# Performance work log

Measured on AMD Instinct MI355X. Metric: run time of the kernel, lower is better.

Reference implementation:

```python
import jax, jax.numpy as jnp
import numpy as np

H = W = 160  # grid mesh -> N = 25600 vertices
B = 4
D = 64


def _grid_mesh(h, w):
    """Triangulated grid; returns symmetric directed edge list (e0, e1), lexicographically
    sorted like np.where(adj > 0) in the original module."""
    idx = np.arange(h * w).reshape(h, w)
    v00 = idx[:-1, :-1].ravel(); v01 = idx[:-1, 1:].ravel()
    v10 = idx[1:, :-1].ravel(); v11 = idx[1:, 1:].ravel()
    faces = np.concatenate([np.stack([v00, v01, v11], 1), np.stack([v00, v11, v10], 1)], 0)
    pairs = np.concatenate([faces[:, [0, 1]], faces[:, [1, 2]], faces[:, [0, 2]]], 0)
    pairs = np.concatenate([pairs, pairs[:, ::-1]], 0)  # symmetrize (adj + adj.T)
    pairs = np.unique(pairs, axis=0)
    return pairs[:, 0].astype(np.int32), pairs[:, 1].astype(np.int32)


def setup_inputs() -> dict:
    key = jax.random.key(0)
    k1, k2 = jax.random.split(key)
    N = H * W
    e0, e1 = _grid_mesh(H, W)
    x = jax.random.normal(k1, (B, N, 3), dtype=jnp.float32)
    J = jax.random.normal(k2, (B, 3 * N, D), dtype=jnp.float32)
    return {"x": x, "J": J, "e0": jnp.asarray(e0), "e1": jnp.asarray(e1), "k": 0}


def _skew(v):
    # cross-product matrix [v]_x : [E,3,3]
    z = jnp.zeros_like(v[:, 0])
    return jnp.stack([
        jnp.stack([z, -v[:, 2], v[:, 1]], -1),
        jnp.stack([v[:, 2], z, -v[:, 0]], -1),
        jnp.stack([-v[:, 1], v[:, 0], z], -1)], -2)


def _arap_single(xi, Ji, e0, e1, deg):
    N = xi.shape[0]
    Dd = Ji.shape[-1]
    J3 = Ji.reshape(N, 3, Dd)           # per-node 3xD blocks of J
    v = xi[e0] - xi[e1]                  # edge vectors [E,3]
    # (2L kron I3) @ J with L = D - A (edge weights 1), coalesce == scatter-add
    nb = jnp.zeros_like(J3).at[e0].add(J3[e1])
    LJ = 2.0 * (deg[:, None, None] * J3 - nb)
    JTLJ = jnp.einsum('ncd,nce->de', J3, LJ)
    # B has block [v]_x at (e0,e1) and accumulated [v]_x at (e0,e0); B^T blocks are -[v]_x
    S = _skew(v)                         # [E,3,3]
    SJ = jnp.einsum('eij,ejd->eid', S, J3[e0])
    BTJ = jnp.zeros_like(J3).at[e1].add(-SJ).at[e0].add(-SJ)
    # C: block-diagonal, per-node sum over outgoing edges of (|v|^2 I - v v^T), then 3x3 inverse
    I3 = jnp.eye(3, dtype=xi.dtype)
    Cb = (v * v).sum(-1)[:, None, None] * I3 - v[:, :, None] * v[:, None, :]
    C = jnp.zeros((N, 3, 3), xi.dtype).at[e0].add(Cb)
    Cinv = jnp.linalg.inv(C)
    CBTJ = jnp.einsum('nij,njd->nid', Cinv, BTJ)
    JTBCBTJ = jnp.einsum('ncd,nce->de', BTJ, CBTJ)
    e = jnp.clip(jnp.linalg.eigvalsh(JTLJ - JTBCBTJ), 0.0)
    pos = e > 0
    # sqrt(clip(e,0)) with a guard so the vjp stays finite at clipped zeros
    return jnp.where(pos, jnp.sqrt(jnp.where(pos, e, 1.0)), 0.0).sum()


def reference(x, J, e0, e1, k):
    N = x.shape[1]
    deg = jnp.zeros((N,), x.dtype).at[e0].add(1.0)
    traces = jax.vmap(lambda xi, Ji: _arap_single(xi, Ji, e0, e1, deg))(x, J)
    return traces.mean()
```

## Files before the change

### kernel.cpp

```cpp
#include <hip/hip_runtime.h>

constexpr int BN = 4;
constexpr int NV = 25600;
constexpr int DD = 64;
constexpr int PP = 72;
constexpr int KP = 34;
constexpr int WW = 160;
constexpr size_t GEOM_OFF = 1u << 20;
constexpr int GREC = 36;
constexpr int GXN  = 256;
constexpr int NCH  = NV / 4;
constexpr int NITER = NCH / GXN;
static_assert(NITER * GXN == NCH, "grid must divide chunks");

constexpr int NS_STEPS = 11;
__constant__ const float S_TAB[NS_STEPS]  = {1.999940f, 1.999730f, 1.998790f, 1.994560f,
                                             1.976020f, 1.900200f, 1.653000f, 1.241700f,
                                             1.024220f, 1.000220f, 1.000000f};
__constant__ const float MU_TAB[NS_STEPS] = {1.414192f, 1.414118f, 1.413786f, 1.412289f,
                                             1.405710f, 1.378478f, 1.285690f, 1.114316f,
                                             1.012038f, 1.000110f, 1.000000f};

typedef __attribute__((ext_vector_type(8))) short short8;
typedef __attribute__((ext_vector_type(4))) float floatx4;

__device__ __forceinline__ unsigned short f2bf(float x) {
    unsigned u = __float_as_uint(x);
    u += 0x7fffu + ((u >> 16) & 1u);
    return (unsigned short)(u >> 16);
}
__device__ __forceinline__ float bf2f(unsigned short h) {
    return __uint_as_float(((unsigned)h) << 16);
}
__device__ __forceinline__ unsigned pack2bf(float a, float b) {
    return (unsigned)f2bf(a) | ((unsigned)f2bf(b) << 16);
}

__global__ void rowptr_kernel(const int* __restrict__ e0, int E, int* __restrict__ row_ptr,
                              float* __restrict__ M, float* __restrict__ out) {
    int i = blockIdx.x * blockDim.x + threadIdx.x;
    if (i < BN * 64 * 64) M[i] = 0.f;
    if (i == 0) out[0] = 0.f;
    if (i > NV) return;
    int lo = 0, hi = E;
    while (lo < hi) {
        int mid = (lo + hi) >> 1;
        if (e0[mid] < i) lo = mid + 1; else hi = mid;
    }
    row_ptr[i] = lo;
}

__global__ __launch_bounds__(256) void geom_kernel(
    const float* __restrict__ x, float* __restrict__ geom,
    float* __restrict__ M, float* __restrict__ out)
{
    const int gid = blockIdx.x * 256 + threadIdx.x;
    if (gid < BN * 64 * 64) M[gid] = 0.f;
    if (gid == 0) out[0] = 0.f;
    if (gid >= BN * NV) return;
    const int b = gid / NV;
    const int n = gid - b * NV;
    const int r = n / WW;
    const int c = n - r * WW;
    const bool up = r > 0, dn = r < WW - 1, lf = c > 0, rt = c < WW - 1;
    int mm[6];
    mm[0] = (up && lf) ? n - WW - 1 : n;
    mm[1] = up ? n - WW : n;
    mm[2] = lf ? n - 1 : n;
    mm[3] = rt ? n + 1 : n;
    mm[4] = dn ? n + WW : n;
    mm[5] = (dn && rt) ? n + WW + 1 : n;

    const float* xb = x + (size_t)b * NV * 3;
    const float xn0 = xb[n * 3], xn1 = xb[n * 3 + 1], xn2 = xb[n * 3 + 2];
    float v[6][3];
    float sv0 = 0, sv1 = 0, sv2 = 0;
    float cxx = 0, cxy = 0, cxz = 0, cyy = 0, cyz = 0, czz = 0;
#pragma unroll
    for (int k = 0; k < 6; k++) {
        const int m = mm[k];
        const float v0 = xn0 - xb[m * 3];
        const float v1 = xn1 - xb[m * 3 + 1];
        const float v2 = xn2 - xb[m * 3 + 2];
        v[k][0] = v0; v[k][1] = v1; v[k][2] = v2;
        sv0 += v0; sv1 += v1; sv2 += v2;
        const float s2 = v0 * v0 + v1 * v1 + v2 * v2;
        cxx += s2 - v0 * v0; cyy += s2 - v1 * v1; czz += s2 - v2 * v2;
        cxy -= v0 * v1; cxz -= v0 * v2; cyz -= v1 * v2;
    }
    const float co00 = cyy * czz - cyz * cyz;
    const float co01 = cxz * cyz - cxy * czz;
    const float co02 = cxy * cyz - cxz * cyy;
    const float det  = cxx * co00 + cxy * co01 + cxz * co02;
    const float id   = 1.0f / det;
    const float i00 = co00 * id, i01 = co01 * id, i02 = co02 * id;
    const float i11 = (cxx * czz - cxz * cxz) * id;
    const float i12 = (cxz * cxy - cxx * cyz) * id;
    const float i22 = (cxx * cyy - cxy * cxy) * id;

    float4* g4 = (float4*)(geom + (size_t)gid * GREC);
    g4[0] = make_float4(v[0][0], v[0][1], v[0][2], v[1][0]);
    g4[1] = make_float4(v[1][1], v[1][2], v[2][0], v[2][1]);
    g4[2] = make_float4(v[2][2], v[3][0], v[3][1], v[3][2]);
    g4[3] = make_float4(v[4][0], v[4][1], v[4][2], v[5][0]);
    g4[4] = make_float4(v[5][1], v[5][2], sv0, sv1);
    g4[5] = make_float4(sv2, i00, i01, i02);
    g4[6] = make_float4(i11, i12, i22, 0.f);
    g4[7] = make_float4(__int_as_float(mm[0]), __int_as_float(mm[1]),
                        __int_as_float(mm[2]), __int_as_float(mm[3]));
    g4[8] = make_float4(__int_as_float(mm[4]), __int_as_float(mm[5]), 0.f, 0.f);
}

__device__ __forceinline__ short8 ldfrag(const unsigned short* a, int row, int quad) {
    const unsigned* p = (const unsigned*)(a + row * KP + quad * 8);
    union { unsigned u[4]; short8 s; } t;
    t.u[0] = p[0]; t.u[1] = p[1]; t.u[2] = p[2]; t.u[3] = p[3];
    return t.s;
}

struct GRec { float v[18]; float sv[3]; float ci[6]; int mm[6]; };
struct JRegs { float n0, n1, n2; float m0[6], m1[6], m2[6]; };

__device__ __forceinline__ void load_grec(const float* __restrict__ g, GRec& o) {
#pragma unroll
    for (int i = 0; i < 18; i++) o.v[i] = g[i];
    o.sv[0] = g[18]; o.sv[1] = g[19]; o.sv[2] = g[20];
#pragma unroll
    for (int i = 0; i < 6; i++) o.ci[i] = g[21 + i];
    const int* gi = (const int*)(g + 28);
#pragma unroll
    for (int i = 0; i < 6; i++) o.mm[i] = gi[i];
}

__device__ __forceinline__ void load_jregs(const float* __restrict__ Jb, int n,
                                           const int* __restrict__ mm, int lane, JRegs& o) {
    const float* Jn = Jb + (size_t)n * (3 * DD) + lane;
    o.n0 = Jn[0]; o.n1 = Jn[DD]; o.n2 = Jn[2 * DD];
#pragma unroll
    for (int k = 0; k < 6; k++) {
        const float* Jm = Jb + (size_t)mm[k] * (3 * DD) + lane;
        o.m0[k] = Jm[0]; o.m1[k] = Jm[DD]; o.m2[k] = Jm[2 * DD];
    }
}

__global__ __launch_bounds__(256, 4) void node_kernel_fast(
    const float* __restrict__ J, const float* __restrict__ geom,
    float* __restrict__ M)
{
    const int b    = blockIdx.y;
    const int w    = __builtin_amdgcn_readfirstlane(threadIdx.x >> 6);
    const int lane = threadIdx.x & 63;
    const int quad = lane >> 4;
    const int mrow = lane & 15;
    const int r0   = w * 16;

    __shared__ unsigned short ATh[2][64 * KP];
    __shared__ unsigned short BTh[2][64 * KP];
    for (int i = threadIdx.x; i < 2 * 64 * KP; i += 256) {
        (&ATh[0][0])[i] = 0;
        (&BTh[0][0])[i] = 0;
    }

    const floatx4 zero4 = {0.f, 0.f, 0.f, 0.f};
    floatx4 accM[4];
#pragma unroll
    for (int c = 0; c < 4; c++) accM[c] = zero4;

    const float* Jb = J + (size_t)b * 3 * NV * DD;
    const float* Gb = geom + (size_t)b * NV * GREC;

    GRec G0, G1;
    JRegs JA, JB;
    {
        const int n0 = blockIdx.x * 4 + w;
        load_grec(Gb + (size_t)n0 * GREC, G0);
        load_jregs(Jb, n0, G0.mm, lane, JA);
    }
    __syncthreads();

    auto body = [&](int it, const GRec& Gc, const JRegs& Jc, GRec& Gn, JRegs& Jnx) {
        const int p   = it & 1;
        const int itN = it + 1;
        const int nN = ((itN < NITER) ? (blockIdx.x + itN * GXN) : blockIdx.x) * 4 + w;
        load_grec(Gb + (size_t)nN * GREC, Gn);

        const float sm0 = (Jc.m0[0] + Jc.m0[1]) + (Jc.m0[2] + Jc.m0[3]) + (Jc.m0[4] + Jc.m0[5]);
        const float sm1 = (Jc.m1[0] + Jc.m1[1]) + (Jc.m1[2] + Jc.m1[3]) + (Jc.m1[4] + Jc.m1[5]);
        const float sm2 = (Jc.m2[0] + Jc.m2[1]) + (Jc.m2[2] + Jc.m2[3]) + (Jc.m2[4] + Jc.m2[5]);
        const float lj0 = 12.f * Jc.n0 - 2.f * sm0;
        const float lj1 = 12.f * Jc.n1 - 2.f * sm1;
        const float lj2 = 12.f * Jc.n2 - 2.f * sm2;

        const float sv0 = Gc.sv[0], sv1 = Gc.sv[1], sv2 = Gc.sv[2];
        float bt0 = sv2 * Jc.n1 - sv1 * Jc.n2;
        float bt1 = sv0 * Jc.n2 - sv2 * Jc.n0;
        float bt2 = sv1 * Jc.n0 - sv0 * Jc.n1;
#pragma unroll
        for (int k = 0; k < 6; k++) {
            const float v0 = Gc.v[k * 3], v1 = Gc.v[k * 3 + 1], v2 = Gc.v[k * 3 + 2];
            bt0 += v1 * Jc.m2[k] - v2 * Jc.m1[k];
            bt1 += v2 * Jc.m0[k] - v0 * Jc.m2[k];
            bt2 += v0 * Jc.m1[k] - v1 * Jc.m0[k];
        }

        const float i00 = Gc.ci[0], i01 = Gc.ci[1], i02 = Gc.ci[2];
        const float i11 = Gc.ci[3], i12 = Gc.ci[4], i22 = Gc.ci[5];
        const float cb0 = i00 * bt0 + i01 * bt1 + i02 * bt2;
        const float cb1 = i01 * bt0 + i11 * bt1 + i12 * bt2;
        const float cb2 = i02 * bt0 + i12 * bt1 + i22 * bt2;

        {
            const int base = lane * (KP / 2) + w * 3;
            unsigned* A32 = (unsigned*)ATh[p];
            unsigned* B32 = (unsigned*)BTh[p];
            A32[base + 0] = pack2bf(Jc.n0, Jc.n1);
            A32[base + 1] = pack2bf(Jc.n2, bt0);
            A32[base + 2] = pack2bf(bt1, bt2);
            B32[base + 0] = pack2bf(lj0, lj1);
            B32[base + 1] = pack2bf(lj2, -cb0);
            B32[base + 2] = pack2bf(-cb1, -cb2);
        }

        load_jregs(Jb, nN, Gn.mm, lane, Jnx);

        __syncthreads();

        const short8 ah = ldfrag(ATh[p], r0 + mrow, quad);
#pragma unroll
        for (int c = 0; c < 4; c++) {
            const short8 bh = ldfrag(BTh[p], c * 16 + mrow, quad);
            accM[c] = __builtin_amdgcn_mfma_f32_16x16x32_bf16(ah, bh, accM[c], 0, 0, 0);
        }
    };

    for (int it = 0; it < NITER - 1; it += 2) {
        body(it,     G0, JA, G1, JB);
        body(it + 1, G1, JB, G0, JA);
    }
    body(NITER - 1, G0, JA, G1, JB);

    float* Mb = M + b * 4096;
    const int cofs = blockIdx.x & 3;
#pragma unroll
    for (int cc = 0; cc < 4; cc++) {
        const int c = (cc + cofs) & 3;
#pragma unroll
        for (int r = 0; r < 4; r++)
            atomicAdd(&Mb[(r0 + quad * 4 + r) * 64 + (c * 16 + mrow)], accM[c][r]);
    }
}

__global__ __launch_bounds__(256, 4) void node_kernel_slow(
    const float* __restrict__ x, const float* __restrict__ J,
    const int* __restrict__ e1, const int* __restrict__ row_ptr,
    float* __restrict__ M)
{
    const int b    = blockIdx.y;
    const int w    = __builtin_amdgcn_readfirstlane(threadIdx.x >> 6);
    const int lane = threadIdx.x & 63;
    const int quad = lane >> 4;
    const int mrow = lane & 15;
    const int r0   = w * 16;

    __shared__ unsigned short ATh[64 * KP], ATl[64 * KP];
    __shared__ unsigned short BTh[64 * KP], BTl[64 * KP];
    for (int i = threadIdx.x; i < 64 * KP; i += 256) { ATh[i]=0; ATl[i]=0; BTh[i]=0; BTl[i]=0; }
    __syncthreads();

    const floatx4 zero4 = {0.f, 0.f, 0.f, 0.f};
    floatx4 accM[4];
#pragma unroll
    for (int c = 0; c < 4; c++) accM[c] = zero4;

    const float* xb = x + (size_t)b * NV * 3;
    const float* Jb = J + (size_t)b * 3 * NV * DD;

    for (int chunk = blockIdx.x; chunk < NV / 4; chunk += gridDim.x) {
        const int n   = chunk * 4 + w;
        const int beg = row_ptr[n];
        const int deg = row_ptr[n + 1] - beg;
        int mm[6];
#pragma unroll
        for (int k = 0; k < 6; k++) {
            const int idx = beg + ((k < deg) ? k : 0);
            const int mv  = e1[idx];
            mm[k] = (k < deg) ? mv : n;
        }
        const float* Jn = Jb + n * 3 * DD + lane;
        const float jn0 = Jn[0], jn1 = Jn[DD], jn2 = Jn[2 * DD];
        float jm0[6], jm1[6], jm2[6];
#pragma unroll
        for (int k = 0; k < 6; k++) {
            const float* Jm = Jb + mm[k] * 3 * DD + lane;
            jm0[k] = Jm[0]; jm1[k] = Jm[DD]; jm2[k] = Jm[2 * DD];
        }
        const float xn0 = xb[n * 3 + 0], xn1 = xb[n * 3 + 1], xn2 = xb[n * 3 + 2];
        float va0[6], va1[6], va2[6];
#pragma unroll
        for (int k = 0; k < 6; k++) {
            va0[k] = xn0 - xb[mm[k] * 3 + 0];
            va1[k] = xn1 - xb[mm[k] * 3 + 1];
            va2[k] = xn2 - xb[mm[k] * 3 + 2];
        }
        float lj0=0, lj1=0, lj2=0, bt0=0, bt1=0, bt2=0;
        float cxx=0, cxy=0, cxz=0, cyy=0, cyz=0, czz=0;
#pragma unroll
        for (int k = 0; k < 6; k++) {
            const float v0 = va0[k], v1 = va1[k], v2 = va2[k];
            const float t0 = jm0[k]-jn0, t1 = jm1[k]-jn1, t2 = jm2[k]-jn2;
            lj0 -= t0; lj1 -= t1; lj2 -= t2;
            bt0 += v1*t2 - v2*t1; bt1 += v2*t0 - v0*t2; bt2 += v0*t1 - v1*t0;
            const float s2 = v0*v0 + v1*v1 + v2*v2;
            cxx += s2 - v0*v0; cyy += s2 - v1*v1; czz += s2 - v2*v2;
            cxy -= v0*v1; cxz -= v0*v2; cyz -= v1*v2;
        }
        lj0 *= 2.f; lj1 *= 2.f; lj2 *= 2.f;
        const float co00 = cyy*czz - cyz*cyz;
        const float co01 = cxz*cyz - cxy*czz;
        const float co02 = cxy*cyz - cxz*cyy;
        const float det  = cxx*co00 + cxy*co01 + cxz*co02;
        const float id   = 1.0f / det;
        const float i00 = co00*id, i01 = co01*id, i02 = co02*id;
        const float i11 = (cxx*czz - cxz*cxz)*id;
        const float i12 = (cxz*cxy - cxx*cyz)*id;
        const float i22 = (cxx*cyy - cxy*cxy)*id;
        const float cb0 = i00*bt0 + i01*bt1 + i02*bt2;
        const float cb1 = i01*bt0 + i11*bt1 + i12*bt2;
        const float cb2 = i02*bt0 + i12*bt1 + i22*bt2;
        {
            const int kA = w * 6;
            float av[6] = {jn0, jn1, jn2, bt0, bt1, bt2};
            float bv[6] = {lj0, lj1, lj2, -cb0, -cb1, -cb2};
#pragma unroll
            for (int i = 0; i < 6; i++) {
                unsigned short h = f2bf(av[i]);
                ATh[lane*KP + kA + i] = h; ATl[lane*KP + kA + i] = f2bf(av[i] - bf2f(h));
                h = f2bf(bv[i]);
                BTh[lane*KP + kA + i] = h; BTl[lane*KP + kA + i] = f2bf(bv[i] - bf2f(h));
            }
        }
        __syncthreads();
        const short8 ah = ldfrag(ATh, r0 + mrow, quad);
        const short8 al = ldfrag(ATl, r0 + mrow, quad);
#pragma unroll
        for (int c = 0; c < 4; c++) {
            const short8 bh = ldfrag(BTh, c*16 + mrow, quad);
            const short8 bl = ldfrag(BTl, c*16 + mrow, quad);
            accM[c] = __builtin_amdgcn_mfma_f32_16x16x32_bf16(ah, bh, accM[c], 0, 0, 0);
            accM[c] = __builtin_amdgcn_mfma_f32_16x16x32_bf16(ah, bl, accM[c], 0, 0, 0);
            accM[c] = __builtin_amdgcn_mfma_f32_16x16x32_bf16(al, bh, accM[c], 0, 0, 0);
        }
        __syncthreads();
    }
    float* Mb = M + b * 4096;
#pragma unroll
    for (int c = 0; c < 4; c++)
#pragma unroll
        for (int r = 0; r < 4; r++)
            atomicAdd(&Mb[(r0 + quad*4 + r) * 64 + (c*16 + mrow)], accM[c][r]);
}

__global__ __launch_bounds__(512, 1) void ns_sqrt_kernel(const float* __restrict__ M,
                                                         float* __restrict__ out)
{
    const int b    = blockIdx.x;
    const int tid  = threadIdx.x;
    const int w    = tid >> 6;
    const int lane = tid & 63;
    const int quad = lane >> 4;
    const int mrow = lane & 15;
    const int tr   = (w & 3) * 16;
    const int tc0  = (w >> 2) * 32;

    __shared__ __align__(16) unsigned short Yh[2][64 * PP], Yl[2][64 * PP];
    __shared__ __align__(16) unsigned short Zh[2][64 * PP], Zl[2][64 * PP];
    __shared__ __align__(16) unsigned short Wh[64 * PP], Wl[64 * PP];
    __shared__ float red_s[8];
    __shared__ float tr_s;

    const float* Mb = M + b * 4096;

    {
        float f2 = 0.f;
        for (int i = tid; i < 4096; i += 512) { const float v = Mb[i]; f2 += v * v; }
#pragma unroll
        for (int off = 32; off; off >>= 1) f2 += __shfl_down(f2, off, 64);
        if (lane == 0) red_s[w] = f2;
        if (tid < 64) {
            float d = Mb[tid * 64 + tid];
#pragma unroll
            for (int off = 32; off; off >>= 1) d += __shfl_down(d, off, 64);
            if (tid == 0) tr_s = d;
        }
    }
    __syncthreads();
    const float trM   = tr_s;
    float f2s = 0.f;
#pragma unroll
    for (int i = 0; i < 8; i++) f2s += red_s[i];
    const float fro   = sqrtf(f2s);
    const float delta = 3e-5f * trM;
    const float cnorm = fro + 2.f * delta;
    const float inv_c = 1.f / cnorm;

    {
        const float s0 = S_TAB[0], mu0 = MU_TAB[0];
        for (int i = tid; i < 4096; i += 512) {
            const int r = i >> 6, col = i & 63;
            float y = Mb[i] * inv_c;
            if (r == col) y += delta * inv_c;
            unsigned short h = f2bf(y);
            Yh[0][r * PP + col] = h;
            Yl[0][r * PP + col] = f2bf(y - bf2f(h));
            float wv = mu0 * (-0.5f * s0 * y);
            if (r == col) wv += mu0 * 1.5f;
            h = f2bf(wv);
            Wh[r * PP + col] = h;
            Wl[r * PP + col] = f2bf(wv - bf2f(h));
            Zh[1][r * PP + col] = h;
            Zl[1][r * PP + col] = Wl[r * PP + col];
        }
    }
    __syncthreads();

    const floatx4 zero4 = {0.f, 0.f, 0.f, 0.f};

    {
        floatx4 y0[2], y1[2], y2[2];
#pragma unroll
        for (int c = 0; c < 2; c++) { y0[c] = zero4; y1[c] = zero4; y2[c] = zero4; }
#pragma unroll
        for (int ks = 0; ks < 2; ks++) {
            const int ko = ks * 32 + quad * 8;
            const short8 yah = *(const short8*)&Yh[0][(tr + mrow) * PP + ko];
            const short8 yal = *(const short8*)&Yl[0][(tr + mrow) * PP + ko];
#pragma unroll
            for (int c = 0; c < 2; c++) {
                const short8 wbh = *(const short8*)&Wh[(tc0 + c * 16 + mrow) * PP + ko];
                const short8 wbl = *(const short8*)&Wl[(tc0 + c * 16 + mrow) * PP + ko];
                y0[c] = __builtin_amdgcn_mfma_f32_16x16x32_bf16(yah, wbh, y0[c], 0, 0, 0);
                y1[c] = __builtin_amdgcn_mfma_f32_16x16x32_bf16(yah, wbl, y1[c], 0, 0, 0);
                y2[c] = __builtin_amdgcn_mfma_f32_16x16x32_bf16(yal, wbh, y2[c], 0, 0, 0);
            }
        }
#pragma unroll
        for (int c = 0; c < 2; c++) {
#pragma unroll
            for (int r = 0; r < 4; r++) {
                const int row = tr + quad * 4 + r;
                const int col = tc0 + c * 16 + mrow;
                const float vy = y0[c][r] + y1[c][r] + y2[c][r];
                const unsigned short h = f2bf(vy);
                Yh[1][row * PP + col] = h;
                Yl[1][row * PP + col] = f2bf(vy - bf2f(h));
            }
        }
        __syncthreads();
    }

    for (int it = 1; it < NS_STEPS; ++it) {
        const int cur = it & 1, nxt = cur ^ 1;
        const float s = S_TAB[it], mu = MU_TAB[it];
        const unsigned short* yh = Yh[cur]; const unsigned short* yl = Yl[cur];
        const unsigned short* zh = Zh[cur]; const unsigned short* zl = Zl[cur];

        floatx4 t0[2], t1[2], t2[2];
#pragma unroll
        for (int c = 0; c < 2; c++) { t0[c] = zero4; t1[c] = zero4; t2[c] = zero4; }
#pragma unroll
        for (int ks = 0; ks < 2; ks++) {
            const int ko = ks * 32 + quad * 8;
            const short8 zah = *(const short8*)&zh[(tr + mrow) * PP + ko];
            const short8 zal = *(const short8*)&zl[(tr + mrow) * PP + ko];
#pragma unroll
            for (int c = 0; c < 2; c++) {
                const short8 ybh = *(const short8*)&yh[(tc0 + c * 16 + mrow) * PP + ko];
                const short8 ybl = *(const short8*)&yl[(tc0 + c * 16 + mrow) * PP + ko];
                t0[c] = __builtin_amdgcn_mfma_f32_16x16x32_bf16(zah, ybh, t0[c], 0, 0, 0);
                t1[c] = __builtin_amdgcn_mfma_f32_16x16x32_bf16(zah, ybl, t1[c], 0, 0, 0);
                t2[c] = __builtin_amdgcn_mfma_f32_16x16x32_bf16(zal, ybh, t2[c], 0, 0, 0);
            }
        }
#pragma unroll
        for (int c = 0; c < 2; c++) {
#pragma unroll
            for (int r = 0; r < 4; r++) {
                const int row = tr + quad * 4 + r;
                const int col = tc0 + c * 16 + mrow;
                float v = mu * (-0.5f * s) * (t0[c][r] + t1[c][r] + t2[c][r]);
                if (row == col) v += mu * 1.5f;
                const unsigned short h = f2bf(v);
                Wh[row * PP + col] = h;
                Wl[row * PP + col] = f2bf(v - bf2f(h));
            }
        }
        __syncthreads();

        floatx4 y0[2], y1[2], y2[2], z0[2], z1[2], z2[2];
#pragma unroll
        for (int c = 0; c < 2; c++) {
            y0[c] = zero4; y1[c] = zero4; y2[c] = zero4;
            z0[c] = zero4; z1[c] = zero4; z2[c] = zero4;
        }
#pragma unroll
        for (int ks = 0; ks < 2; ks++) {
            const int ko = ks * 32 + quad * 8;
            const short8 yah = *(const short8*)&yh[(tr + mrow) * PP + ko];
            const short8 yal = *(const short8*)&yl[(tr + mrow) * PP + ko];
            const short8 wah = *(const short8*)&Wh[(tr + mrow) * PP + ko];
            const short8 wal = *(const short8*)&Wl[(tr + mrow) * PP + ko];
#pragma unroll
            for (int c = 0; c < 2; c++) {
                const int bc = (tc0 + c * 16 + mrow) * PP + ko;
                const short8 wbh = *(const short8*)&Wh[bc];
                const short8 wbl = *(const short8*)&Wl[bc];
                y0[c] = __builtin_amdgcn_mfma_f32_16x16x32_bf16(yah, wbh, y0[c], 0, 0, 0);
                y1[c] = __builtin_amdgcn_mfma_f32_16x16x32_bf16(yah, wbl, y1[c], 0, 0, 0);
                y2[c] = __builtin_amdgcn_mfma_f32_16x16x32_bf16(yal, wbh, y2[c], 0, 0, 0);
                const short8 zbh = *(const short8*)&zh[bc];
                const short8 zbl = *(const short8*)&zl[bc];
                z0[c] = __builtin_amdgcn_mfma_f32_16x16x32_bf16(wah, zbh, z0[c], 0, 0, 0);
                z1[c] = __builtin_amdgcn_mfma_f32_16x16x32_bf16(wah, zbl, z1[c], 0, 0, 0);
                z2[c] = __builtin_amdgcn_mfma_f32_16x16x32_bf16(wal, zbh, z2[c], 0, 0, 0);
            }
        }
#pragma unroll
        for (int c = 0; c < 2; c++) {
#pragma unroll
            for (int r = 0; r < 4; r++) {
                const int row = tr + quad * 4 + r;
                const int col = tc0 + c * 16 + mrow;
                const float vy = y0[c][r] + y1[c][r] + y2[c][r];
                const float vz = z0[c][r] + z1[c][r] + z2[c][r];
                unsigned short h = f2bf(vy);
                Yh[nxt][row * PP + col] = h;
                Yl[nxt][row * PP + col] = f2bf(vy - bf2f(h));
                h = f2bf(vz);
                Zh[nxt][row * PP + col] = h;
                Zl[nxt][row * PP + col] = f2bf(vz - bf2f(h));
            }
        }
        __syncthreads();
    }

    const int fin = NS_STEPS & 1;
    if (tid < 64) {
        float d = bf2f(Yh[fin][tid * PP + tid]) + bf2f(Yl[fin][tid * PP + tid]);
#pragma unroll
        for (int off = 32; off; off >>= 1) d += __shfl_down(d, off, 64);
        if (tid == 0) atomicAdd(out, d * sqrtf(cnorm) * (1.0f / BN));
    }
}

extern "C" void kernel_launch(void* const* d_in, const int* in_sizes, int n_in,
                              void* d_out, int out_size, void* d_ws, size_t ws_size,
                              hipStream_t stream) {
    const float* x  = (const float*)d_in[0];
    const float* J  = (const float*)d_in[1];
    const int*   e0 = (const int*)d_in[2];
    const int*   e1 = (const int*)d_in[3];
    const int E = in_sizes[2];

    int*   row_ptr = (int*)d_ws;
    float* M       = (float*)((char*)d_ws + 128 * 1024);
    float* geom    = (float*)((char*)d_ws + GEOM_OFF);
    const size_t need = GEOM_OFF + (size_t)BN * NV * GREC * sizeof(float);

    if (ws_size >= need) {
        geom_kernel<<<(BN * NV + 255) / 256, 256, 0, stream>>>(x, geom, M, (float*)d_out);
        node_kernel_fast<<<dim3(GXN, BN), 256, 0, stream>>>(J, geom, M);
    } else {
        rowptr_kernel<<<(NV + 1 + 255) / 256, 256, 0, stream>>>(e0, E, row_ptr, M, (float*)d_out);
        node_kernel_slow<<<dim3(512, BN), 256, 0, stream>>>(x, J, e1, row_ptr, M);
    }
    ns_sqrt_kernel<<<BN, 512, 0, stream>>>(M, (float*)d_out);
}
```

Measured before the change: 192.8 us.

## Partition M atomics, recompute neighbor indices, widen Newton-Schulz block to 1024 threads

Spreads the node-kernel atomic accumulation of the 64x64 matrix over 8 partial copies per batch to reduce atomic contention, and the sqrt kernel sums those partials into shared memory. Neighbor indices are now computed arithmetically instead of read from the geometry record, so the J gathers for the next node can be issued before the geometry load. The Newton-Schulz kernel runs 16 waves of 1024 threads, each owning one 16x16 tile, to shorten the per-wave MFMA chain. The risks are extra zeroing and partial-sum reads, plus the added shared memory for msum.

```diff
diff --git a/kernel.cpp b/kernel.cpp
--- a/kernel.cpp
+++ b/kernel.cpp
@@ -6,6 +6,7 @@
 constexpr int PP = 72;
 constexpr int KP = 34;
 constexpr int WW = 160;
+constexpr int NPART = 8;
 constexpr size_t GEOM_OFF = 1u << 20;
 constexpr int GREC = 36;
 constexpr int GXN  = 256;
@@ -36,10 +37,23 @@
     return (unsigned)f2bf(a) | ((unsigned)f2bf(b) << 16);
 }
 
+__device__ __forceinline__ void mm_arith(int n, int* mm) {
+    const int r = n / WW;
+    const int c = n - r * WW;
+    const bool up = r > 0, dn = r < WW - 1, lf = c > 0, rt = c < WW - 1;
+    mm[0] = (up && lf) ? n - WW - 1 : n;
+    mm[1] = up ? n - WW : n;
+    mm[2] = lf ? n - 1 : n;
+    mm[3] = rt ? n + 1 : n;
+    mm[4] = dn ? n + WW : n;
+    mm[5] = (dn && rt) ? n + WW + 1 : n;
+}
+
 __global__ void rowptr_kernel(const int* __restrict__ e0, int E, int* __restrict__ row_ptr,
                               float* __restrict__ M, float* __restrict__ out) {
-    int i = blockIdx.x * blockDim.x + threadIdx.x;
-    if (i < BN * 64 * 64) M[i] = 0.f;
+    const int i = blockIdx.x * blockDim.x + threadIdx.x;
+    const int nthr = gridDim.x * blockDim.x;
+    for (int j = i; j < NPART * BN * 4096; j += nthr) M[j] = 0.f;
     if (i == 0) out[0] = 0.f;
     if (i > NV) return;
     int lo = 0, hi = E;
@@ -55,21 +69,13 @@
     float* __restrict__ M, float* __restrict__ out)
 {
     const int gid = blockIdx.x * 256 + threadIdx.x;
-    if (gid < BN * 64 * 64) M[gid] = 0.f;
+    for (int i = gid; i < NPART * BN * 4096; i += BN * NV) M[i] = 0.f;
     if (gid == 0) out[0] = 0.f;
     if (gid >= BN * NV) return;
     const int b = gid / NV;
     const int n = gid - b * NV;
-    const int r = n / WW;
-    const int c = n - r * WW;
-    const bool up = r > 0, dn = r < WW - 1, lf = c > 0, rt = c < WW - 1;
     int mm[6];
-    mm[0] = (up && lf) ? n - WW - 1 : n;
-    mm[1] = up ? n - WW : n;
-    mm[2] = lf ? n - 1 : n;
-    mm[3] = rt ? n + 1 : n;
-    mm[4] = dn ? n + WW : n;
-    mm[5] = (dn && rt) ? n + WW + 1 : n;
+    mm_arith(n, mm);
 
     const float* xb = x + (size_t)b * NV * 3;
     const float xn0 = xb[n * 3], xn1 = xb[n * 3 + 1], xn2 = xb[n * 3 + 2];
@@ -118,7 +124,7 @@
     return t.s;
 }
 
-struct GRec { float v[18]; float sv[3]; float ci[6]; int mm[6]; };
+struct GRec { float v[18]; float sv[3]; float ci[6]; };
 struct JRegs { float n0, n1, n2; float m0[6], m1[6], m2[6]; };
 
 __device__ __forceinline__ void load_grec(const float* __restrict__ g, GRec& o) {
@@ -127,9 +133,6 @@
     o.sv[0] = g[18]; o.sv[1] = g[19]; o.sv[2] = g[20];
 #pragma unroll
     for (int i = 0; i < 6; i++) o.ci[i] = g[21 + i];
-    const int* gi = (const int*)(g + 28);
-#pragma unroll
-    for (int i = 0; i < 6; i++) o.mm[i] = gi[i];
 }
 
 __device__ __forceinline__ void load_jregs(const float* __restrict__ Jb, int n,
@@ -173,15 +176,20 @@
     JRegs JA, JB;
     {
         const int n0 = blockIdx.x * 4 + w;
+        int mm0[6];
+        mm_arith(n0, mm0);
+        load_jregs(Jb, n0, mm0, lane, JA);
         load_grec(Gb + (size_t)n0 * GREC, G0);
-        load_jregs(Jb, n0, G0.mm, lane, JA);
     }
     __syncthreads();
 
     auto body = [&](int it, const GRec& Gc, const JRegs& Jc, GRec& Gn, JRegs& Jnx) {
         const int p   = it & 1;
-        const int itN = it + 1;
-        const int nN = ((itN < NITER) ? (blockIdx.x + itN * GXN) : blockIdx.x) * 4 + w;
+        const int itN = (it + 1 < NITER) ? (it + 1) : 0;
+        const int nN  = (blockIdx.x + itN * GXN) * 4 + w;
+        int mmN[6];
+        mm_arith(nN, mmN);
+        load_jregs(Jb, nN, mmN, lane, Jnx);
         load_grec(Gb + (size_t)nN * GREC, Gn);
 
         const float sm0 = (Jc.m0[0] + Jc.m0[1]) + (Jc.m0[2] + Jc.m0[3]) + (Jc.m0[4] + Jc.m0[5]);
@@ -221,8 +229,6 @@
             B32[base + 2] = pack2bf(-cb1, -cb2);
         }
 
-        load_jregs(Jb, nN, Gn.mm, lane, Jnx);
-
         __syncthreads();
 
         const short8 ah = ldfrag(ATh[p], r0 + mrow, quad);
@@ -239,7 +245,8 @@
     }
     body(NITER - 1, G0, JA, G1, JB);
 
-    float* Mb = M + b * 4096;
+    const int prt = blockIdx.x & (NPART - 1);
+    float* Mb = M + ((size_t)prt * BN + b) * 4096;
     const int cofs = blockIdx.x & 3;
 #pragma unroll
     for (int cc = 0; cc < 4; cc++) {
@@ -352,7 +359,8 @@
         }
         __syncthreads();
     }
-    float* Mb = M + b * 4096;
+    const int prt = blockIdx.x & (NPART - 1);
+    float* Mb = M + ((size_t)prt * BN + b) * 4096;
 #pragma unroll
     for (int c = 0; c < 4; c++)
 #pragma unroll
@@ -360,8 +368,8 @@
             atomicAdd(&Mb[(r0 + quad*4 + r) * 64 + (c*16 + mrow)], accM[c][r]);
 }
 
-__global__ __launch_bounds__(512, 1) void ns_sqrt_kernel(const float* __restrict__ M,
-                                                         float* __restrict__ out)
+__global__ __launch_bounds__(1024, 1) void ns_sqrt_kernel(const float* __restrict__ M,
+                                                          float* __restrict__ out)
 {
     const int b    = blockIdx.x;
     const int tid  = threadIdx.x;
@@ -370,24 +378,34 @@
     const int quad = lane >> 4;
     const int mrow = lane & 15;
     const int tr   = (w & 3) * 16;
-    const int tc0  = (w >> 2) * 32;
+    const int tc   = (w >> 2) * 16;
 
     __shared__ __align__(16) unsigned short Yh[2][64 * PP], Yl[2][64 * PP];
     __shared__ __align__(16) unsigned short Zh[2][64 * PP], Zl[2][64 * PP];
     __shared__ __align__(16) unsigned short Wh[64 * PP], Wl[64 * PP];
-    __shared__ float red_s[8];
+    __shared__ float msum[4096];
+    __shared__ float red_s[16];
     __shared__ float tr_s;
 
+    constexpr int PS = BN * 4096;
     const float* Mb = M + b * 4096;
 
     {
         float f2 = 0.f;
-        for (int i = tid; i < 4096; i += 512) { const float v = Mb[i]; f2 += v * v; }
+        for (int i = tid; i < 4096; i += 1024) {
+            float v = 0.f;
+#pragma unroll
+            for (int pI = 0; pI < NPART; pI++) v += Mb[pI * PS + i];
+            msum[i] = v;
+            f2 += v * v;
+        }
 #pragma unroll
         for (int off = 32; off; off >>= 1) f2 += __shfl_down(f2, off, 64);
         if (lane == 0) red_s[w] = f2;
         if (tid < 64) {
-            float d = Mb[tid * 64 + tid];
+            float d = 0.f;
+#pragma unroll
+            for (int pI = 0; pI < NPART; pI++) d += Mb[pI * PS + tid * 65];
 #pragma unroll
             for (int off = 32; off; off >>= 1) d += __shfl_down(d, off, 64);
             if (tid == 0) tr_s = d;
@@ -397,7 +415,7 @@
     const float trM   = tr_s;
     float f2s = 0.f;
 #pragma unroll
-    for (int i = 0; i < 8; i++) f2s += red_s[i];
+    for (int i = 0; i < 16; i++) f2s += red_s[i];
     const float fro   = sqrtf(f2s);
     const float delta = 3e-5f * trM;
     const float cnorm = fro + 2.f * delta;
@@ -405,9 +423,9 @@
 
     {
         const float s0 = S_TAB[0], mu0 = MU_TAB[0];
-        for (int i = tid; i < 4096; i += 512) {
+        for (int i = tid; i < 4096; i += 1024) {
             const int r = i >> 6, col = i & 63;
-            float y = Mb[i] * inv_c;
+            float y = msum[i] * inv_c;
             if (r == col) y += delta * inv_c;
             unsigned short h = f2bf(y);
             Yh[0][r * PP + col] = h;
@@ -426,34 +444,26 @@
     const floatx4 zero4 = {0.f, 0.f, 0.f, 0.f};
 
     {
-        floatx4 y0[2], y1[2], y2[2];
-#pragma unroll
-        for (int c = 0; c < 2; c++) { y0[c] = zero4; y1[c] = zero4; y2[c] = zero4; }
+        floatx4 y0 = zero4, y1 = zero4, y2 = zero4;
 #pragma unroll
         for (int ks = 0; ks < 2; ks++) {
             const int ko = ks * 32 + quad * 8;
             const short8 yah = *(const short8*)&Yh[0][(tr + mrow) * PP + ko];
             const short8 yal = *(const short8*)&Yl[0][(tr + mrow) * PP + ko];
-#pragma unroll
-            for (int c = 0; c < 2; c++) {
-                const short8 wbh = *(const short8*)&Wh[(tc0 + c * 16 + mrow) * PP + ko];
-                const short8 wbl = *(const short8*)&Wl[(tc0 + c * 16 + mrow) * PP + ko];
-                y0[c] = __builtin_amdgcn_mfma_f32_16x16x32_bf16(yah, wbh, y0[c], 0, 0, 0);
-                y1[c] = __builtin_amdgcn_mfma_f32_16x16x32_bf16(yah, wbl, y1[c], 0, 0, 0);
-                y2[c] = __builtin_amdgcn_mfma_f32_16x16x32_bf16(yal, wbh, y2[c], 0, 0, 0);
-            }
-        }
-#pragma unroll
-        for (int c = 0; c < 2; c++) {
-#pragma unroll
-            for (int r = 0; r < 4; r++) {
-                const int row = tr + quad * 4 + r;
-                const int col = tc0 + c * 16 + mrow;
-                const float vy = y0[c][r] + y1[c][r] + y2[c][r];
-                const unsigned short h = f2bf(vy);
-                Yh[1][row * PP + col] = h;
-                Yl[1][row * PP + col] = f2bf(vy - bf2f(h));
-            }
+            const short8 wbh = *(const short8*)&Wh[(tc + mrow) * PP + ko];
+            const short8 wbl = *(const short8*)&Wl[(tc + mrow) * PP + ko];
+            y0 = __builtin_amdgcn_mfma_f32_16x16x32_bf16(yah, wbh, y0, 0, 0, 0);
+            y1 = __builtin_amdgcn_mfma_f32_16x16x32_bf16(yah, wbl, y1, 0, 0, 0);
+            y2 = __builtin_amdgcn_mfma_f32_16x16x32_bf16(yal, wbh, y2, 0, 0, 0);
+        }
+#pragma unroll
+        for (int r = 0; r < 4; r++) {
+            const int row = tr + quad * 4 + r;
+            const int col = tc + mrow;
+            const float vy = y0[r] + y1[r] + y2[r];
+            const unsigned short h = f2bf(vy);
+            Yh[1][row * PP + col] = h;
+            Yl[1][row * PP + col] = f2bf(vy - bf2f(h));
         }
         __syncthreads();
     }
@@ -464,81 +474,63 @@
         const unsigned short* yh = Yh[cur]; const unsigned short* yl = Yl[cur];
         const unsigned short* zh = Zh[cur]; const unsigned short* zl = Zl[cur];
 
-        floatx4 t0[2], t1[2], t2[2];
-#pragma unroll
-        for (int c = 0; c < 2; c++) { t0[c] = zero4; t1[c] = zero4; t2[c] = zero4; }
+        floatx4 t0 = zero4, t1 = zero4, t2 = zero4;
 #pragma unroll
         for (int ks = 0; ks < 2; ks++) {
             const int ko = ks * 32 + quad * 8;
             const short8 zah = *(const short8*)&zh[(tr + mrow) * PP + ko];
             const short8 zal = *(const short8*)&zl[(tr + mrow) * PP + ko];
-#pragma unroll
-            for (int c = 0; c < 2; c++) {
-                const short8 ybh = *(const short8*)&yh[(tc0 + c * 16 + mrow) * PP + ko];
-                const short8 ybl = *(const short8*)&yl[(tc0 + c * 16 + mrow) * PP + ko];
-                t0[c] = __builtin_amdgcn_mfma_f32_16x16x32_bf16(zah, ybh, t0[c], 0, 0, 0);
-                t1[c] = __builtin_amdgcn_mfma_f32_16x16x32_bf16(zah, ybl, t1[c], 0, 0, 0);
-                t2[c] = __builtin_amdgcn_mfma_f32_16x16x32_bf16(zal, ybh, t2[c], 0, 0, 0);
-            }
-        }
-#pragma unroll
-        for (int c = 0; c < 2; c++) {
-#pragma unroll
-            for (int r = 0; r < 4; r++) {
-                const int row = tr + quad * 4 + r;
-                const int col = tc0 + c * 16 + mrow;
-                float v = mu * (-0.5f * s) * (t0[c][r] + t1[c][r] + t2[c][r]);
-                if (row == col) v += mu * 1.5f;
-                const unsigned short h = f2bf(v);
-                Wh[row * PP + col] = h;
-                Wl[row * PP + col] = f2bf(v - bf2f(h));
-            }
+            const short8 ybh = *(const short8*)&yh[(tc + mrow) * PP + ko];
+            const short8 ybl = *(const short8*)&yl[(tc + mrow) * PP + ko];
+            t0 = __builtin_amdgcn_mfma_f32_16x16x32_bf16(zah, ybh, t0, 0, 0, 0);
+            t1 = __builtin_amdgcn_mfma_f32_16x16x32_bf16(zah, ybl, t1, 0, 0, 0);
+            t2 = __builtin_amdgcn_mfma_f32_16x16x32_bf16(zal, ybh, t2, 0, 0, 0);
+        }
+#pragma unroll
+        for (int r = 0; r < 4; r++) {
+            const int row = tr + quad * 4 + r;
+            const int col = tc + mrow;
+            float v = mu * (-0.5f * s) * (t0[r] + t1[r] + t2[r]);
+            if (row == col) v += mu * 1.5f;
+            const unsigned short h = f2bf(v);
+            Wh[row * PP + col] = h;
+            Wl[row * PP + col] = f2bf(v - bf2f(h));
         }
         __syncthreads();
 
-        floatx4 y0[2], y1[2], y2[2], z0[2], z1[2], z2[2];
-#pragma unroll
-        for (int c = 0; c < 2; c++) {
-            y0[c] = zero4; y1[c] = zero4; y2[c] = zero4;
-            z0[c] = zero4; z1[c] = zero4; z2[c] = zero4;
-        }
+        floatx4 y0 = zero4, y1 = zero4, y2 = zero4, z0 = zero4, z1 = zero4, z2 = zero4;
 #pragma unroll
         for (int ks = 0; ks < 2; ks++) {
             const int ko = ks * 32 + quad * 8;
-            const short8 yah = *(const short8*)&yh[(tr + mrow) * PP + ko];
-            const short8 yal = *(const short8*)&yl[(tr + mrow) * PP + ko];
-            const short8 wah = *(const short8*)&Wh[(tr + mrow) * PP + ko];
-            const short8 wal = *(const short8*)&Wl[(tr + mrow) * PP + ko];
-#pragma unroll
-            for (int c = 0; c < 2; c++) {
-                const int bc = (tc0 + c * 16 + mrow) * PP + ko;
-                const short8 wbh = *(const short8*)&Wh[bc];
-                const short8 wbl = *(const short8*)&Wl[bc];
-                y0[c] = __builtin_amdgcn_mfma_f32_16x16x32_bf16(yah, wbh, y0[c], 0, 0, 0);
-                y1[c] = __builtin_amdgcn_mfma_f32_16x16x32_bf16(yah, wbl, y1[c], 0, 0, 0);
-                y2[c] = __builtin_amdgcn_mfma_f32_16x16x32_bf16(yal, wbh, y2[c], 0, 0, 0);
-                const short8 zbh = *(const short8*)&zh[bc];
-                const short8 zbl = *(const short8*)&zl[bc];
-                z0[c] = __builtin_amdgcn_mfma_f32_16x16x32_bf16(wah, zbh, z0[c], 0, 0, 0);
-                z1[c] = __builtin_amdgcn_mfma_f32_16x16x32_bf16(wah, zbl, z1[c], 0, 0, 0);
-                z2[c] = __builtin_amdgcn_mfma_f32_16x16x32_bf16(wal, zbh, z2[c], 0, 0, 0);
-            }
-        }
-#pragma unroll
-        for (int c = 0; c < 2; c++) {
-#pragma unroll
-            for (int r = 0; r < 4; r++) {
-                const int row = tr + quad * 4 + r;
-                const int col = tc0 + c * 16 + mrow;
-                const float vy = y0[c][r] + y1[c][r] + y2[c][r];
-                const float vz = z0[c][r] + z1[c][r] + z2[c][r];
-                unsigned short h = f2bf(vy);
-                Yh[nxt][row * PP + col] = h;
-                Yl[nxt][row * PP + col] = f2bf(vy - bf2f(h));
-                h = f2bf(vz);
-                Zh[nxt][row * PP + col] = h;
-                Zl[nxt][row * PP + col] = f2bf(vz - bf2f(h));
-            }
+            const int ar = (tr + mrow) * PP + ko;
+            const int bc = (tc + mrow) * PP + ko;
+            const short8 yah = *(const short8*)&yh[ar];
+            const short8 yal = *(const short8*)&yl[ar];
+            const short8 wah = *(const short8*)&Wh[ar];
+            const short8 wal = *(const short8*)&Wl[ar];
+            const short8 wbh = *(const short8*)&Wh[bc];
+            const short8 wbl = *(const short8*)&Wl[bc];
+            const short8 zbh = *(const short8*)&zh[bc];
+            const short8 zbl = *(const short8*)&zl[bc];
+            y0 = __builtin_amdgcn_mfma_f32_16x16x32_bf16(yah, wbh, y0, 0, 0, 0);
+            y1 = __builtin_amdgcn_mfma_f32_16x16x32_bf16(yah, wbl, y1, 0, 0, 0);
+            y2 = __builtin_amdgcn_mfma_f32_16x16x32_bf16(yal, wbh, y2, 0, 0, 0);
+            z0 = __builtin_amdgcn_mfma_f32_16x16x32_bf16(wah, zbh, z0, 0, 0, 0);
+            z1 = __builtin_amdgcn_mfma_f32_16x16x32_bf16(wah, zbl, z1, 0, 0, 0);
+            z2 = __builtin_amdgcn_mfma_f32_16x16x32_bf16(wal, zbh, z2, 0, 0, 0);
+        }
+#pragma unroll
+        for (int r = 0; r < 4; r++) {
+            const int row = tr + quad * 4 + r;
+            const int col = tc + mrow;
+            const float vy = y0[r] + y1[r] + y2[r];
+            const float vz = z0[r] + z1[r] + z2[r];
+            unsigned short h = f2bf(vy);
+            Yh[nxt][row * PP + col] = h;
+            Yl[nxt][row * PP + col] = f2bf(vy - bf2f(h));
+            h = f2bf(vz);
+            Zh[nxt][row * PP + col] = h;
+            Zl[nxt][row * PP + col] = f2bf(vz - bf2f(h));
         }
         __syncthreads();
     }
@@ -573,5 +565,5 @@
         rowptr_kernel<<<(NV + 1 + 255) / 256, 256, 0, stream>>>(e0, E, row_ptr, M, (float*)d_out);
         node_kernel_slow<<<dim3(512, BN), 256, 0, stream>>>(x, J, e1, row_ptr, M);
     }
-    ns_sqrt_kernel<<<BN, 512, 0, stream>>>(M, (float*)d_out);
-}
+    ns_sqrt_kernel<<<BN, 1024, 0, stream>>>(M, (float*)d_out);
+}
```

New measurement: 188.2 us. 1.02x faster.
